# Kernel optimization log

Measured on AMD Instinct MI355X. Metric: run time of the kernel, lower is better.

The kernel has to match this reference:

```python
import jax, jax.numpy as jnp
import numpy as np

LN_EPS = 1e-5

def _layer_norm(x, g, b):
    mu = jnp.mean(x, axis=-1, keepdims=True)
    var = jnp.mean(jnp.square(x - mu), axis=-1, keepdims=True)
    return (x - mu) * jax.lax.rsqrt(var + LN_EPS) * g + b

def setup_inputs() -> dict:
    key = jax.random.key(0)
    ks = jax.random.split(key, 12)
    B, L, E, H, W = 4, 1024, 1024, 16, 128
    s = 0.02
    return {
        "x": jax.random.normal(ks[0], (B, L, E), dtype=jnp.float32),
        "in_proj_w": jax.random.normal(ks[1], (3 * E, E), dtype=jnp.float32) * s,
        "in_proj_b": jnp.zeros((3 * E,), dtype=jnp.float32),
        "out_proj_w": jax.random.normal(ks[2], (E, E), dtype=jnp.float32) * s,
        "out_proj_b": jnp.zeros((E,), dtype=jnp.float32),
        "ln1_g": jnp.ones((E,), dtype=jnp.float32),
        "ln1_b": jnp.zeros((E,), dtype=jnp.float32),
        "w1": jax.random.normal(ks[3], (4 * E, E), dtype=jnp.float32) * s,
        "b1": jnp.zeros((4 * E,), dtype=jnp.float32),
        "w2": jax.random.normal(ks[4], (E, 4 * E), dtype=jnp.float32) * s,
        "b2": jnp.zeros((E,), dtype=jnp.float32),
        "ln2_g": jnp.ones((E,), dtype=jnp.float32),
        "ln2_b": jnp.zeros((E,), dtype=jnp.float32),
        "n_head": 16,
        "window_size": 128,
    }

def reference(x, in_proj_w, in_proj_b, out_proj_w, out_proj_b,
              ln1_g, ln1_b, w1, b1, w2, b2, ln2_g, ln2_b,
              n_head, window_size):
    B, L, E = x.shape
    H = n_head
    D = E // H
    # qkv projection (torch Linear convention: y = x @ W.T + b)
    qkv = jnp.einsum('ble,fe->blf', x, in_proj_w) + in_proj_b  # [B,L,3E]
    q, k, v = jnp.split(qkv, 3, axis=-1)
    q = q.reshape(B, L, H, D).transpose(0, 2, 1, 3)  # [B,H,L,D]
    k = k.reshape(B, L, H, D).transpose(0, 2, 1, 3)
    v = v.reshape(B, L, H, D).transpose(0, 2, 1, 3)
    scores = jnp.einsum('bhld,bhmd->bhlm', q, k) / np.sqrt(D)  # [B,H,L,L]
    # banded window mask: allowed iff |i-j| <= window_size (same as the double loop)
    idx = jnp.arange(L)
    band = jnp.abs(idx[:, None] - idx[None, :]) <= window_size  # [L,L]
    scores = jnp.where(band[None, None], scores, -jnp.inf)
    attn = jax.nn.softmax(scores, axis=-1)  # [B,H,L,L]
    ctx = jnp.einsum('bhlm,bhmd->bhld', attn, v)  # [B,H,L,D]
    ctx = ctx.transpose(0, 2, 1, 3).reshape(B, L, E)
    attn_out = jnp.einsum('ble,fe->blf', ctx, out_proj_w) + out_proj_b
    attn_weights = jnp.mean(attn, axis=1)  # torch MHA averages heads -> [B,L,L]
    # residual + norm1 (dropout is identity in eval)
    h = _layer_norm(x + attn_out, ln1_g, ln1_b)
    # positionwise FFN
    ff = jnp.einsum('ble,fe->blf', h, w1) + b1
    ff = jax.nn.relu(ff)
    ff = jnp.einsum('blf,ef->ble', ff, w2) + b2
    out = _layer_norm(h + ff, ln2_g, ln2_b)
    return (out, attn_weights)
```

## Files before the change

### kernel.cpp

```cpp
#include <hip/hip_runtime.h>

#define BB 4
#define LL 1024
#define EE 1024
#define HH 16
#define DD 64

typedef __attribute__((ext_vector_type(8))) short short8;
typedef __attribute__((ext_vector_type(4))) float floatx4;

#define PSTR ((size_t)4096 * 1024)

__device__ __forceinline__ float bf2f(short s) {
    union { unsigned u; float f; } c;
    c.u = ((unsigned)(unsigned short)s) << 16;
    return c.f;
}
__device__ __forceinline__ short f2bf(float f) {
    union { float f; unsigned u; } c; c.f = f;
    unsigned r = c.u + 0x7fffu + ((c.u >> 16) & 1u);
    return (short)(r >> 16);
}

__device__ __forceinline__ void async_copy16(const void* g, void* l) {
    __builtin_amdgcn_global_load_lds(
        (const __attribute__((address_space(1))) unsigned int*)g,
        (__attribute__((address_space(3))) unsigned int*)l, 16, 0, 0);
}

__global__ __launch_bounds__(256) void cvt5(
    const float* __restrict__ x, const float* __restrict__ wqkv,
    const float* __restrict__ wo, const float* __restrict__ w1,
    const float* __restrict__ w2,
    short* __restrict__ xb, short* __restrict__ wqkvb, short* __restrict__ wob,
    short* __restrict__ w1b, short* __restrict__ w2b)
{
    int bi = blockIdx.x;
    const float* in; short* out; int base;
    if      (bi <  4096) { in = x;    out = xb;    base = 0;     }
    else if (bi <  7168) { in = wqkv; out = wqkvb; base = 4096;  }
    else if (bi <  8192) { in = wo;   out = wob;   base = 7168;  }
    else if (bi < 12288) { in = w1;   out = w1b;   base = 8192;  }
    else                 { in = w2;   out = w2b;   base = 12288; }
    int i = (bi - base) * 256 + threadIdx.x;
    float4 v = ((const float4*)in)[i];
    unsigned long long u =
          (unsigned long long)(unsigned short)f2bf(v.x)
        | ((unsigned long long)(unsigned short)f2bf(v.y) << 16)
        | ((unsigned long long)(unsigned short)f2bf(v.z) << 32)
        | ((unsigned long long)(unsigned short)f2bf(v.w) << 48);
    ((unsigned long long*)out)[i] = u;
}

template<bool RELU, bool WVT, bool SK>
__global__ __launch_bounds__(256) void gemm_bt(
    const short* __restrict__ A, const short* __restrict__ Bw,
    const float* __restrict__ bias,
    short* __restrict__ Cb, short* __restrict__ VTp,
    int M, int N, int K, int Ksp)
{
    __shared__ union U {
        struct { short As[128 * 64]; short Bs[128 * 64]; } s;
        short Cs[128 * 136];
    } u;
    const int tid  = threadIdx.x;
    const int wave = tid >> 6, lane = tid & 63;
    const int m0 = blockIdx.x * 128, n0 = blockIdx.y * 128;
    const int wm = (wave & 1) * 64, wn = (wave >> 1) * 64;
    const int kbase = SK ? blockIdx.z * Ksp : 0;

    floatx4 acc[4][4];
#pragma unroll
    for (int i = 0; i < 4; ++i)
#pragma unroll
        for (int j = 0; j < 4; ++j) acc[i][j] = (floatx4){0.f, 0.f, 0.f, 0.f};

    const int srow = wave * 8 + (lane >> 3);
    const int scol = (((lane & 7) ^ ((lane >> 3) & 7))) * 8;
    const short* gA = A  + (size_t)(m0 + srow) * K + kbase + scol;
    const short* gB = Bw + (size_t)(n0 + srow) * K + kbase + scol;
    short* lA = u.s.As + wave * 512;
    short* lB = u.s.Bs + wave * 512;

    const int fr = lane & 15, quad = lane >> 4;
    const int kiters = (SK ? Ksp : K) >> 6;
    for (int kt = 0; kt < kiters; ++kt) {
#pragma unroll
        for (int s = 0; s < 4; ++s) {
            async_copy16(gA + (size_t)s * 32 * K, lA + s * 2048);
            async_copy16(gB + (size_t)s * 32 * K, lB + s * 2048);
        }
        gA += 64; gB += 64;
        __syncthreads();
#pragma unroll
        for (int ks = 0; ks < 2; ++ks) {
            short8 af[4], bf[4];
#pragma unroll
            for (int i = 0; i < 4; ++i) {
                int pos = ((ks * 4 + quad) ^ (fr & 7)) * 8;
                af[i] = *(const short8*)&u.s.As[(wm + i * 16 + fr) * 64 + pos];
                bf[i] = *(const short8*)&u.s.Bs[(wn + i * 16 + fr) * 64 + pos];
            }
#pragma unroll
            for (int i = 0; i < 4; ++i)
#pragma unroll
                for (int j = 0; j < 4; ++j)
                    acc[i][j] = __builtin_amdgcn_mfma_f32_16x16x32_bf16(af[i], bf[j], acc[i][j], 0, 0, 0);
        }
        __syncthreads();
    }

    const int cc = lane & 15;
    const int rb = (lane >> 4) * 4;
#pragma unroll
    for (int j = 0; j < 4; ++j) {
        int col = wn + j * 16 + cc;
        float bv = SK ? 0.0f : bias[n0 + col];
#pragma unroll
        for (int i = 0; i < 4; ++i) {
            int row = wm + i * 16 + rb;
#pragma unroll
            for (int r = 0; r < 4; ++r) {
                float v = acc[i][j][r] + bv;
                if (RELU) v = fmaxf(v, 0.0f);
                u.Cs[(row + r) * 136 + col] = f2bf(v);
            }
        }
    }
    __syncthreads();
    short* Co = Cb + (SK ? (size_t)blockIdx.z * PSTR : 0);
    const int trow = tid >> 4, tcol = (tid & 15) * 8;
#pragma unroll
    for (int p = 0; p < 8; ++p) {
        int row = p * 16 + trow;
        short8 vv = *(const short8*)&u.Cs[row * 136 + tcol];
        *(short8*)&Co[(size_t)(m0 + row) * N + n0 + tcol] = vv;
        if (WVT) {
            int gc0 = n0 + tcol;
            if (gc0 >= 2048) {
                int tok = m0 + row;
                int hc = (gc0 - 2048) >> 6, d0 = (gc0 - 2048) & 63;
                short* vrow = VTp + ((size_t)((tok >> 10) * 16 + hc) * 64 + d0) * 1024 + (tok & 1023);
#pragma unroll
                for (int e = 0; e < 8; ++e) vrow[(size_t)e * 1024] = vv[e];
            }
        }
    }
}

__global__ __launch_bounds__(256) void ln_kernel(
    const float* __restrict__ xa, const short* __restrict__ parts, int nparts,
    const float* __restrict__ bias,
    const float* __restrict__ g, const float* __restrict__ beta,
    float* __restrict__ outf, short* __restrict__ outb)
{
    const int row = blockIdx.x;
    const int tid = threadIdx.x;
    float4 va = ((const float4*)(xa + (size_t)row * EE))[tid];
    float4 vb = ((const float4*)bias)[tid];
    float v0 = va.x + vb.x, v1 = va.y + vb.y, v2 = va.z + vb.z, v3 = va.w + vb.w;
#pragma unroll 4
    for (int p = 0; p < nparts; ++p) {
        unsigned long long u8 = ((const unsigned long long*)(parts + p * PSTR + (size_t)row * EE))[tid];
        v0 += bf2f((short)(u8 & 0xffff));
        v1 += bf2f((short)((u8 >> 16) & 0xffff));
        v2 += bf2f((short)((u8 >> 32) & 0xffff));
        v3 += bf2f((short)(u8 >> 48));
    }
    float s  = v0 + v1 + v2 + v3;
    float ss = v0 * v0 + v1 * v1 + v2 * v2 + v3 * v3;
#pragma unroll
    for (int o = 1; o < 64; o <<= 1) { s += __shfl_xor(s, o); ss += __shfl_xor(ss, o); }
    __shared__ float red[8];
    if ((tid & 63) == 0) { red[(tid >> 6) * 2] = s; red[(tid >> 6) * 2 + 1] = ss; }
    __syncthreads();
    s  = red[0] + red[2] + red[4] + red[6];
    ss = red[1] + red[3] + red[5] + red[7];
    float mean = s * (1.0f / EE);
    float var  = ss * (1.0f / EE) - mean * mean;
    float rstd = rsqrtf(var + 1e-5f);
    float4 vg = ((const float4*)g)[tid];
    float4 vt = ((const float4*)beta)[tid];
    float o0 = (v0 - mean) * rstd * vg.x + vt.x;
    float o1 = (v1 - mean) * rstd * vg.y + vt.y;
    float o2 = (v2 - mean) * rstd * vg.z + vt.z;
    float o3 = (v3 - mean) * rstd * vg.w + vt.w;
    if (outf) ((float4*)(outf + (size_t)row * EE))[tid] = make_float4(o0, o1, o2, o3);
    if (outb) {
        unsigned long long u =
              (unsigned long long)(unsigned short)f2bf(o0)
            | ((unsigned long long)(unsigned short)f2bf(o1) << 16)
            | ((unsigned long long)(unsigned short)f2bf(o2) << 32)
            | ((unsigned long long)(unsigned short)f2bf(o3) << 48);
        ((unsigned long long*)(outb + (size_t)row * EE))[tid] = u;
    }
}

__global__ __launch_bounds__(512, 8) void attn_mfma(
    const short* __restrict__ qkv,
    const short* __restrict__ vt,
    short* __restrict__ ctxp,
    short* __restrict__ pb)
{
    __shared__ short Pl[32 * 320];
    __shared__ float Red[4][2][32];
    const int tid = threadIdx.x, wave = tid >> 6, lane = tid & 63;
    const int quad = lane >> 4, mcol = lane & 15;
    const int id = blockIdx.x;
    const int i0 = (id >> 6) * 32, h = id & 15, b = (id >> 4) & 3;
    const int jb0 = i0 - 128;

    const short* qb = qkv + (size_t)(b * 1024) * 3072 + h * 64;
    const short* kb = qb + 1024;

    const int mt = wave >> 2, qtr = wave & 3;
    const short* qrow = qb + (size_t)(i0 + mt * 16 + mcol) * 3072 + quad * 8;
    short8 aq0 = *(const short8*)qrow;
    short8 aq1 = *(const short8*)(qrow + 32);

    floatx4 sacc[5];
#pragma unroll
    for (int c = 0; c < 5; ++c) sacc[c] = (floatx4){0.f, 0.f, 0.f, 0.f};
#pragma unroll
    for (int c = 0; c < 5; ++c) {
        int j = jb0 + (qtr * 5 + c) * 16 + mcol;
        j = min(max(j, 0), 1023);
        const short* kr = kb + (size_t)j * 3072 + quad * 8;
        short8 b0 = *(const short8*)kr;
        short8 b1 = *(const short8*)(kr + 32);
        sacc[c] = __builtin_amdgcn_mfma_f32_16x16x32_bf16(aq0, b0, sacc[c], 0, 0, 0);
        sacc[c] = __builtin_amdgcn_mfma_f32_16x16x32_bf16(aq1, b1, sacc[c], 0, 0, 0);
    }

    const int row0 = mt * 16 + quad * 4;
#pragma unroll
    for (int r = 0; r < 4; ++r) {
        int row = row0 + r;
        float m = -1e30f;
#pragma unroll
        for (int c = 0; c < 5; ++c) {
            int jo = (qtr * 5 + c) * 16 + mcol;
            bool val = (jo >= row) && (jo <= row + 256) && ((unsigned)(jb0 + jo) < 1024u);
            float s = val ? sacc[c][r] * 0.125f : -1e30f;
            sacc[c][r] = s;
            m = fmaxf(m, s);
        }
        m = fmaxf(m, __shfl_xor(m, 1));
        m = fmaxf(m, __shfl_xor(m, 2));
        m = fmaxf(m, __shfl_xor(m, 4));
        m = fmaxf(m, __shfl_xor(m, 8));
        if (mcol == 0) Red[qtr][0][row] = m;
    }
    __syncthreads();
#pragma unroll
    for (int r = 0; r < 4; ++r) {
        int row = row0 + r;
        float M = fmaxf(fmaxf(Red[0][0][row], Red[1][0][row]),
                        fmaxf(Red[2][0][row], Red[3][0][row]));
        float l = 0.f;
#pragma unroll
        for (int c = 0; c < 5; ++c) {
            float p = __expf(sacc[c][r] - M);
            sacc[c][r] = p;
            l += p;
        }
        l += __shfl_xor(l, 1);
        l += __shfl_xor(l, 2);
        l += __shfl_xor(l, 4);
        l += __shfl_xor(l, 8);
        if (mcol == 0) Red[qtr][1][row] = l;
    }
    __syncthreads();
#pragma unroll
    for (int r = 0; r < 4; ++r) {
        int row = row0 + r;
        float inv = 1.0f / (Red[0][1][row] + Red[1][1][row] +
                            Red[2][1][row] + Red[3][1][row]);
#pragma unroll
        for (int c = 0; c < 5; ++c) {
            int jo = (qtr * 5 + c) * 16 + mcol;
            Pl[row * 320 + (((jo >> 3) ^ (row & 7)) * 8) + (jo & 7)] = f2bf(sacc[c][r] * inv);
        }
    }
    __syncthreads();

    const int pmt = wave & 1, dt = wave >> 1;
    floatx4 cacc = (floatx4){0.f, 0.f, 0.f, 0.f};
    const short* vrow = vt + ((size_t)((b * 16 + h) * 64) + dt * 16 + mcol) * 1024;
    const int prow = (pmt * 16 + mcol) * 320;
#pragma unroll
    for (int jc = 0; jc < 10; ++jc) {
        short8 ap = *(const short8*)&Pl[prow + (((jc * 4 + quad) ^ (mcol & 7)) * 8)];
        int jg = jb0 + jc * 32 + quad * 8;
        if ((unsigned)jg >= 1024u) jg = 0;
        short8 bv = *(const short8*)(vrow + jg);
        cacc = __builtin_amdgcn_mfma_f32_16x16x32_bf16(ap, bv, cacc, 0, 0, 0);
    }

    short* pbb = pb + ((size_t)((b * 16 + h) * 1024) + i0) * 320;
    for (int t = tid; t < 1280; t += 512) {
        int row = t / 40, c = t - row * 40;
        short8 v = *(const short8*)&Pl[row * 320 + ((c ^ (row & 7)) * 8)];
        *(short8*)&pbb[(size_t)t * 8] = v;
    }
    __syncthreads();

    short* Ct = Pl;
    const int colc = dt * 16 + mcol;
#pragma unroll
    for (int r = 0; r < 4; ++r)
        Ct[(pmt * 16 + quad * 4 + r) * 72 + colc] = f2bf(cacc[r]);
    __syncthreads();
    short* cb = ctxp + (size_t)(b * 1024 + i0) * 1024 + h * 64;
    for (int t = tid; t < 256; t += 512) {
        int row = t >> 3, c = t & 7;
        short8 v = *(const short8*)&Ct[row * 72 + c * 8];
        *(short8*)&cb[(size_t)row * 1024 + c * 8] = v;
    }
}

__global__ __launch_bounds__(256) void pb_reduce(const short* __restrict__ pb,
                                                 float* __restrict__ aw)
{
    const int i = blockIdx.x & 1023, b = blockIdx.x >> 10;
    const int i0 = i & ~31;
    __shared__ short P[16 * 320];
    for (int t = threadIdx.x; t < 640; t += 256) {
        int hh = t / 40, c = t - hh * 40;
        ((short8*)P)[t] = *(const short8*)(pb +
            ((size_t)((b * 16 + hh) * 1024) + i) * 320 + c * 8);
    }
    __syncthreads();
    float* row = aw + ((size_t)(b * 1024) + i) * 1024;
    for (int j = threadIdx.x; j < 1024; j += 256) {
        int jo = j - i0 + 128;
        float s = 0.f;
        if ((unsigned)jo < 320u) {
#pragma unroll
            for (int hh = 0; hh < 16; ++hh)
                s += bf2f(P[hh * 320 + jo]);
            s *= (1.0f / 16.0f);
        }
        row[j] = s;
    }
}

extern "C" void kernel_launch(void* const* d_in, const int* in_sizes, int n_in,
                              void* d_out, int out_size, void* d_ws, size_t ws_size,
                              hipStream_t stream) {
    const float* x    = (const float*)d_in[0];
    const float* wqkv = (const float*)d_in[1];
    const float* bqkv = (const float*)d_in[2];
    const float* wo   = (const float*)d_in[3];
    const float* bo   = (const float*)d_in[4];
    const float* g1   = (const float*)d_in[5];
    const float* be1  = (const float*)d_in[6];
    const float* w1   = (const float*)d_in[7];
    const float* bb1  = (const float*)d_in[8];
    const float* w2   = (const float*)d_in[9];
    const float* bb2  = (const float*)d_in[10];
    const float* g2   = (const float*)d_in[11];
    const float* be2  = (const float*)d_in[12];

    char* ws = (char*)d_ws;
    size_t off = 0;
    auto take = [&](size_t bytes) {
        void* p = ws + off;
        off += (bytes + 255) & ~(size_t)255;
        return p;
    };
    short* xb     = (short*)take((size_t)4096 * 1024 * 2);
    short* wqkv_b = (short*)take((size_t)3072 * 1024 * 2);
    short* wo_b   = (short*)take((size_t)1024 * 1024 * 2);
    short* w1_b   = (short*)take((size_t)4096 * 1024 * 2);
    short* w2_b   = (short*)take((size_t)1024 * 4096 * 2);
    short* qkv_b  = (short*)take((size_t)4096 * 3072 * 2);
    short* ctx_b  = (short*)take((size_t)4096 * 1024 * 2);
    short* ff2_p  = qkv_b;
    short* attn_p = (short*)take((size_t)2 * 4096 * 1024 * 2);
    float* h_f    = (float*)take((size_t)4096 * 1024 * 4);
    short* vt_ws  = (short*)h_f;
    short* h_b    = (short*)take((size_t)4096 * 1024 * 2);
    short* pb_ws  = (short*)take((size_t)4 * 16 * 1024 * 320 * 2);
    short* ff_b   = pb_ws;

    float* out_f = (float*)d_out;
    float* attnW = (float*)d_out + (size_t)4 * 1024 * 1024;

    cvt5<<<16384, 256, 0, stream>>>(x, wqkv, wo, w1, w2, xb, wqkv_b, wo_b, w1_b, w2_b);

    gemm_bt<false, true, false><<<dim3(32, 24), 256, 0, stream>>>(
        xb, wqkv_b, bqkv, qkv_b, vt_ws, 4096, 3072, 1024, 1024);

    attn_mfma<<<2048, 512, 0, stream>>>(qkv_b, vt_ws, ctx_b, pb_ws);

    pb_reduce<<<4096, 256, 0, stream>>>(pb_ws, attnW);

    gemm_bt<false, false, true><<<dim3(32, 8, 2), 256, 0, stream>>>(
        ctx_b, wo_b, nullptr, attn_p, nullptr, 4096, 1024, 1024, 512);

    ln_kernel<<<4096, 256, 0, stream>>>(x, attn_p, 2, bo, g1, be1, h_f, h_b);

    gemm_bt<true, false, false><<<dim3(32, 32), 256, 0, stream>>>(
        h_b, w1_b, bb1, ff_b, nullptr, 4096, 4096, 1024, 1024);

    gemm_bt<false, false, true><<<dim3(32, 8, 4), 256, 0, stream>>>(
        ff_b, w2_b, nullptr, ff2_p, nullptr, 4096, 1024, 4096, 1024);

    ln_kernel<<<4096, 256, 0, stream>>>(h_f, ff2_p, 4, bb2, g2, be2, out_f, nullptr);
}
```

Measured before the change: 353.0 us.

## Add 256x256-tile 8-wave bf16 GEMM with swizzled LDS and block remap

Adds a new GEMM kernel that gives each 512-thread block a 256x256 output tile. It double-buffers 64-wide K slices in LDS through async copies with an XOR-swizzled layout, and interleaves staging of the next slice with MFMA phases under s_setprio. Block indices are remapped in groups of eight to improve L2 locality. The QKV, FFN1 and split-K FFN2 GEMMs switch to it, which raises arithmetic intensity per LDS byte but launches far fewer blocks (192-256 versus 768-1024 before) and uses about 132 KB of shared memory per block, which may limit occupancy and leave CUs idle on a 256-CU part.

```diff
diff --git a/kernel.cpp b/kernel.cpp
--- a/kernel.cpp
+++ b/kernel.cpp
@@ -53,6 +53,160 @@
 }
 
 template<bool RELU, bool WVT, bool SK>
+__global__ __launch_bounds__(512, 2) void gemm256(
+    const short* __restrict__ A, const short* __restrict__ Bw,
+    const float* __restrict__ bias,
+    short* __restrict__ Cb, short* __restrict__ VTp,
+    int M, int N, int K, int Ksp)
+{
+    __shared__ short SH[67584];
+    const int tid  = threadIdx.x;
+    const int w    = tid >> 6, lane = tid & 63;
+    const int fr   = lane & 15, quad = lane >> 4;
+    const int wm   = w >> 2,  wn   = w & 3;
+
+    const int gx   = gridDim.x;
+    const int flat = blockIdx.y * gx + blockIdx.x;
+    const int nwg  = gx * gridDim.y;
+    const int q8   = nwg >> 3;
+    const int swz  = (flat & 7) * q8 + (flat >> 3);
+    const int m0   = (swz % gx) * 256;
+    const int n0   = (swz / gx) * 256;
+
+    const int kb = SK ? blockIdx.z * Ksp : 0;
+    const int NT = (SK ? Ksp : K) >> 6;
+
+    const int srow = w * 16 + (lane >> 3);
+    const int gcol = ((lane & 7) ^ ((lane >> 3) & 7)) * 8;
+
+    auto stage = [&](int s, int h) {
+        if (s >= NT) return;
+        short* dstb = SH + (s & 1) * 32768 + (h >> 1) * 16384 + (h & 1) * 8192 + w * 1024;
+        const short* src = (h < 2)
+            ? A  + (size_t)(m0 + h * 128 + srow) * K + kb + s * 64 + gcol
+            : Bw + (size_t)(n0 + (h - 2) * 128 + srow) * K + kb + s * 64 + gcol;
+        async_copy16(src, dstb);
+        async_copy16(src + (size_t)8 * K, dstb + 512);
+    };
+
+    floatx4 acc[8][4];
+#pragma unroll
+    for (int i = 0; i < 8; ++i)
+#pragma unroll
+        for (int j = 0; j < 4; ++j) acc[i][j] = (floatx4){0.f, 0.f, 0.f, 0.f};
+
+    stage(0, 0); stage(0, 1); stage(0, 2); stage(0, 3);
+    stage(1, 0);
+
+    const int posk0 = ((quad    ) ^ (fr & 7)) * 8;
+    const int posk1 = ((4 + quad) ^ (fr & 7)) * 8;
+
+    for (int t = 0; t < NT; ++t) {
+        if (t < NT - 1) asm volatile("s_waitcnt vmcnt(2)" ::: "memory");
+        else            asm volatile("s_waitcnt vmcnt(0)" ::: "memory");
+        __builtin_amdgcn_sched_barrier(0);
+        __builtin_amdgcn_s_barrier();
+        __builtin_amdgcn_sched_barrier(0);
+
+        const short* sA = SH + (t & 1) * 32768 + wm * 8192;
+        const short* sB = SH + (t & 1) * 32768 + 16384 + wn * 4096;
+
+        short8 aL[4], aH[4], b0[4], b1[4], a2[4], a3[4];
+
+#pragma unroll
+        for (int i = 0; i < 4; ++i) aL[i] = *(const short8*)&sA[(i * 16 + fr) * 64 + posk0];
+#pragma unroll
+        for (int j = 0; j < 4; ++j) b0[j] = *(const short8*)&sB[(j * 16 + fr) * 64 + posk0];
+        stage(t + 1, 1);
+        __builtin_amdgcn_s_setprio(1);
+#pragma unroll
+        for (int i = 0; i < 4; ++i)
+#pragma unroll
+            for (int j = 0; j < 4; ++j)
+                acc[i][j] = __builtin_amdgcn_mfma_f32_16x16x32_bf16(aL[i], b0[j], acc[i][j], 0, 0, 0);
+        __builtin_amdgcn_s_setprio(0);
+
+#pragma unroll
+        for (int i = 0; i < 4; ++i) aH[i] = *(const short8*)&sA[((i + 4) * 16 + fr) * 64 + posk0];
+#pragma unroll
+        for (int j = 0; j < 4; ++j) b1[j] = *(const short8*)&sB[(j * 16 + fr) * 64 + posk1];
+        stage(t + 1, 2);
+        __builtin_amdgcn_s_setprio(1);
+#pragma unroll
+        for (int i = 0; i < 4; ++i)
+#pragma unroll
+            for (int j = 0; j < 4; ++j)
+                acc[i + 4][j] = __builtin_amdgcn_mfma_f32_16x16x32_bf16(aH[i], b0[j], acc[i + 4][j], 0, 0, 0);
+        __builtin_amdgcn_s_setprio(0);
+
+#pragma unroll
+        for (int i = 0; i < 4; ++i) a2[i] = *(const short8*)&sA[(i * 16 + fr) * 64 + posk1];
+#pragma unroll
+        for (int i = 0; i < 4; ++i) a3[i] = *(const short8*)&sA[((i + 4) * 16 + fr) * 64 + posk1];
+        stage(t + 1, 3);
+        __builtin_amdgcn_s_setprio(1);
+#pragma unroll
+        for (int i = 0; i < 4; ++i)
+#pragma unroll
+            for (int j = 0; j < 4; ++j)
+                acc[i][j] = __builtin_amdgcn_mfma_f32_16x16x32_bf16(a2[i], b1[j], acc[i][j], 0, 0, 0);
+        __builtin_amdgcn_s_setprio(0);
+
+        asm volatile("s_waitcnt lgkmcnt(0)" ::: "memory");
+        __builtin_amdgcn_sched_barrier(0);
+        __builtin_amdgcn_s_barrier();
+        __builtin_amdgcn_sched_barrier(0);
+
+        stage(t + 2, 0);
+        __builtin_amdgcn_s_setprio(1);
+#pragma unroll
+        for (int i = 0; i < 4; ++i)
+#pragma unroll
+            for (int j = 0; j < 4; ++j)
+                acc[i + 4][j] = __builtin_amdgcn_mfma_f32_16x16x32_bf16(a3[i], b1[j], acc[i + 4][j], 0, 0, 0);
+        __builtin_amdgcn_s_setprio(0);
+    }
+
+    __syncthreads();
+
+    const int cc = lane & 15, rb4 = quad * 4;
+#pragma unroll
+    for (int i = 0; i < 8; ++i) {
+        int row = wm * 128 + i * 16 + rb4;
+#pragma unroll
+        for (int j = 0; j < 4; ++j) {
+            int col = wn * 64 + j * 16 + cc;
+            float bv = SK ? 0.0f : bias[n0 + col];
+#pragma unroll
+            for (int r = 0; r < 4; ++r) {
+                float v = acc[i][j][r] + bv;
+                if (RELU) v = fmaxf(v, 0.0f);
+                SH[(row + r) * 264 + col] = f2bf(v);
+            }
+        }
+    }
+    __syncthreads();
+    short* Co = Cb + (SK ? (size_t)blockIdx.z * PSTR : 0);
+#pragma unroll
+    for (int it = 0; it < 16; ++it) {
+        int idx = it * 512 + tid;
+        int row = idx >> 5, ch = idx & 31;
+        short8 v = *(const short8*)&SH[row * 264 + ch * 8];
+        *(short8*)&Co[(size_t)(m0 + row) * N + n0 + ch * 8] = v;
+        if (WVT) {
+            int gc0 = n0 + ch * 8;
+            if (gc0 >= 2048) {
+                int tok = m0 + row;
+                int hc = (gc0 - 2048) >> 6, d0 = (gc0 - 2048) & 63;
+                short* vrow = VTp + ((size_t)((tok >> 10) * 16 + hc) * 64 + d0) * 1024 + (tok & 1023);
+#pragma unroll
+                for (int e = 0; e < 8; ++e) vrow[(size_t)e * 1024] = v[e];
+            }
+        }
+    }
+}
+
+template<bool RELU, bool WVT, bool SK>
 __global__ __launch_bounds__(256) void gemm_bt(
     const short* __restrict__ A, const short* __restrict__ Bw,
     const float* __restrict__ bias,
@@ -389,7 +543,7 @@
 
     cvt5<<<16384, 256, 0, stream>>>(x, wqkv, wo, w1, w2, xb, wqkv_b, wo_b, w1_b, w2_b);
 
-    gemm_bt<false, true, false><<<dim3(32, 24), 256, 0, stream>>>(
+    gemm256<false, true, false><<<dim3(16, 12), 512, 0, stream>>>(
         xb, wqkv_b, bqkv, qkv_b, vt_ws, 4096, 3072, 1024, 1024);
 
     attn_mfma<<<2048, 512, 0, stream>>>(qkv_b, vt_ws, ctx_b, pb_ws);
@@ -401,10 +555,10 @@
 
     ln_kernel<<<4096, 256, 0, stream>>>(x, attn_p, 2, bo, g1, be1, h_f, h_b);
 
-    gemm_bt<true, false, false><<<dim3(32, 32), 256, 0, stream>>>(
+    gemm256<true, false, false><<<dim3(16, 16), 512, 0, stream>>>(
         h_b, w1_b, bb1, ff_b, nullptr, 4096, 4096, 1024, 1024);
 
-    gemm_bt<false, false, true><<<dim3(32, 8, 4), 256, 0, stream>>>(
+    gemm256<false, false, true><<<dim3(16, 4, 4), 512, 0, stream>>>(
         ff_b, w2_b, nullptr, ff2_p, nullptr, 4096, 1024, 4096, 1024);
 
     ln_kernel<<<4096, 256, 0, stream>>>(h_f, ff2_p, 4, bb2, g2, be2, out_f, nullptr);
```

New measurement: 349.7 us. About the same (-0.9%).
